# Kernel optimization log

Measured on AMD Instinct MI355X. Metric: run time of the kernel, lower is better.

The kernel has to match this reference:

```python
import jax, jax.numpy as jnp
import numpy as np

B, N, D, H, E = 128, 256, 256, 8, 524288
RATIO = 0.5
HD = D // H
K_SEL = int(N * RATIO)  # nodes kept per graph


def setup_inputs() -> dict:
    key = jax.random.key(0)
    ks = jax.random.split(key, 12)
    embeddings = jax.random.normal(ks[0], (B, N, D), dtype=jnp.float32)
    mask = jnp.ones((B, N), dtype=bool)
    dist = jax.random.uniform(ks[1], (B, N, N), dtype=jnp.float32)
    # within-graph random edges, offset per graph
    epg = E // B
    src = jax.random.randint(ks[2], (B, epg), 0, N)
    dst = jax.random.randint(ks[3], (B, epg), 0, N)
    off = (jnp.arange(B) * N)[:, None]
    edge_index = jnp.stack([(src + off).reshape(-1), (dst + off).reshape(-1)]).astype(jnp.int64)
    batch = jnp.repeat(jnp.arange(B, dtype=jnp.int64), N)
    s = 1.0 / np.sqrt(D)
    Wq = jax.random.normal(ks[4], (D, D), jnp.float32) * s
    Wk = jax.random.normal(ks[5], (D, D), jnp.float32) * s
    Wv = jax.random.normal(ks[6], (D, D), jnp.float32) * s
    Wo = jax.random.normal(ks[7], (D, D), jnp.float32) * s
    bq = jnp.zeros((D,), jnp.float32)
    bk = jnp.zeros((D,), jnp.float32)
    bv = jnp.zeros((D,), jnp.float32)
    bo = jnp.zeros((D,), jnp.float32)
    pool_w = jax.random.normal(ks[8], (D,), jnp.float32) * s
    return dict(embeddings=embeddings, mask=mask, dist=dist, edge_index=edge_index,
                batch=batch, Wq=Wq, bq=bq, Wk=Wk, bk=bk, Wv=Wv, bv=bv, Wo=Wo, bo=bo,
                pool_w=pool_w)


def _mha(x, mask, dist, Wq, bq, Wk, bk, Wv, bv, Wo, bo):
    # x: [B,N,D]; dist used as additive attention bias; mask: [B,N] key mask
    q = (x @ Wq + bq).reshape(B, N, H, HD).transpose(0, 2, 1, 3)  # bhnd
    k = (x @ Wk + bk).reshape(B, N, H, HD).transpose(0, 2, 1, 3)
    v = (x @ Wv + bv).reshape(B, N, H, HD).transpose(0, 2, 1, 3)
    scores = jnp.einsum('bhnd,bhmd->bhnm', q, k) / jnp.sqrt(jnp.float32(HD))
    scores = scores + dist[:, None]  # broadcast bias over heads
    scores = jnp.where(mask[:, None, None, :], scores, jnp.float32(-1e9))
    attn = jax.nn.softmax(scores, axis=-1)
    out = jnp.einsum('bhnm,bhmd->bhnd', attn, v)
    out = out.transpose(0, 2, 1, 3).reshape(B, N, D)
    return out @ Wo + bo


def reference(embeddings, mask, dist, edge_index, batch, Wq, bq, Wk, bk, Wv, bv, Wo, bo, pool_w):
    encoder_result = _mha(embeddings, mask, dist, Wq, bq, Wk, bk, Wv, bv, Wo, bo)
    # encoder_result[mask] -> sparse node features; mask is all-true so shape is [B*N, D]
    x = encoder_result.reshape(B * N, D)

    # ---- TopKPooling (PyG semantics): score = x.w/||w||, keep top ceil(ratio*N)/graph ----
    score = (x @ pool_w) / jnp.linalg.norm(pool_w)          # [B*N]
    vals, idx = jax.lax.top_k(score.reshape(B, N), K_SEL)    # per-graph top-k
    perm = (idx + (jnp.arange(B) * N)[:, None]).reshape(-1)  # [B*K] global node ids
    sub_x = x[perm] * jnp.tanh(vals).reshape(-1, 1)
    sub_batch = batch[perm]

    # relabel nodes: new id = position in perm (PyG ordering); dropped -> sentinel
    n_keep = B * K_SEL
    sentinel = n_keep
    new_id = jnp.full((B * N,), sentinel, dtype=edge_index.dtype).at[perm].set(
        jnp.arange(n_keep, dtype=edge_index.dtype))
    row = new_id[edge_index[0]]
    col = new_id[edge_index[1]]
    valid = (row < sentinel) & (col < sentinel)
    row = jnp.where(valid, row, sentinel)
    col = jnp.where(valid, col, sentinel)
    # sort_edge_index: row-major sort; invalid (sentinel) edges pushed to the end
    order = jnp.argsort(row * (sentinel + 1) + col)
    sub_edge_index = jnp.stack([row, col])[:, order]
    return encoder_result, sub_x, sub_edge_index, sub_batch
```

## Files before the change

### kernel.cpp

```cpp
#include <hip/hip_runtime.h>
#include <math.h>

#define Bg   128
#define Ng   256
#define Dg   256
#define Hg   8
#define HDg  32
#define Eg   524288
#define Kg   128
#define BNg  32768
#define SENT 16384

using bf16x8 = __attribute__((ext_vector_type(8))) short;
using f32x4  = __attribute__((ext_vector_type(4))) float;

__device__ inline void split2(float x, short &h, short &l) {
    unsigned u = __float_as_uint(x);
    h = (short)(u >> 16);
    float hf = __uint_as_float(u & 0xffff0000u);
    float r = x - hf;
    l = (short)(__float_as_uint(r) >> 16);
}
__device__ inline unsigned packsplit(float x) {
    unsigned u = __float_as_uint(x);
    float hf = __uint_as_float(u & 0xffff0000u);
    float r = x - hf;
    unsigned lu = __float_as_uint(r);
    return (u >> 16) | (lu & 0xffff0000u);
}
__device__ inline unsigned pack2(short a, short b) {
    return (unsigned)(unsigned short)a | ((unsigned)(unsigned short)b << 16);
}

__global__ __launch_bounds__(256) void split_x(
    const float* __restrict__ x, short* __restrict__ xh, short* __restrict__ xl)
{
    size_t i = ((size_t)blockIdx.x * 256 + threadIdx.x) * 8;
    float4 a = *(const float4*)(x + i);
    float4 b = *(const float4*)(x + i + 4);
    float v[8] = {a.x,a.y,a.z,a.w,b.x,b.y,b.z,b.w};
    short h[8], l[8];
    #pragma unroll
    for (int j = 0; j < 8; ++j) split2(v[j], h[j], l[j]);
    uint4 uh, ul;
    uh.x = pack2(h[0],h[1]); uh.y = pack2(h[2],h[3]);
    uh.z = pack2(h[4],h[5]); uh.w = pack2(h[6],h[7]);
    ul.x = pack2(l[0],l[1]); ul.y = pack2(l[2],l[3]);
    ul.z = pack2(l[4],l[5]); ul.w = pack2(l[6],l[7]);
    *(uint4*)(xh + i) = uh;
    *(uint4*)(xl + i) = ul;
}

__global__ __launch_bounds__(256) void wprep(
    const float* __restrict__ Wq, const float* __restrict__ Wk,
    const float* __restrict__ Wv, const float* __restrict__ Wo,
    short* __restrict__ WTh, short* __restrict__ WTl)
{
    __shared__ float t[64][65];
    const int bid = blockIdx.x;
    const int mat = bid >> 4;
    const int kt = (bid >> 2) & 3, nt = bid & 3;
    const float* W = (mat==0) ? Wq : (mat==1) ? Wk : (mat==2) ? Wv : Wo;
    const int tid = threadIdx.x;
    const int r = tid >> 2, c4 = tid & 3;
    #pragma unroll
    for (int i = 0; i < 4; ++i) {
        float4 v = *(const float4*)(W + (size_t)(kt*64 + r)*256 + nt*64 + c4*16 + i*4);
        t[r][c4*16 + i*4 + 0] = v.x; t[r][c4*16 + i*4 + 1] = v.y;
        t[r][c4*16 + i*4 + 2] = v.z; t[r][c4*16 + i*4 + 3] = v.w;
    }
    __syncthreads();
    const int n = r, k0 = c4 * 16;
    short hb[16], lb[16];
    #pragma unroll
    for (int i = 0; i < 16; ++i) split2(t[k0 + i][n], hb[i], lb[i]);
    size_t base = (size_t)mat*65536 + (size_t)(nt*64 + n)*256 + kt*64 + k0;
    uint4 uh0, uh1, ul0, ul1;
    uh0.x=pack2(hb[0],hb[1]);  uh0.y=pack2(hb[2],hb[3]);  uh0.z=pack2(hb[4],hb[5]);  uh0.w=pack2(hb[6],hb[7]);
    uh1.x=pack2(hb[8],hb[9]);  uh1.y=pack2(hb[10],hb[11]);uh1.z=pack2(hb[12],hb[13]);uh1.w=pack2(hb[14],hb[15]);
    ul0.x=pack2(lb[0],lb[1]);  ul0.y=pack2(lb[2],lb[3]);  ul0.z=pack2(lb[4],lb[5]);  ul0.w=pack2(lb[6],lb[7]);
    ul1.x=pack2(lb[8],lb[9]);  ul1.y=pack2(lb[10],lb[11]);ul1.z=pack2(lb[12],lb[13]);ul1.w=pack2(lb[14],lb[15]);
    *(uint4*)&WTh[base]     = uh0; *(uint4*)&WTh[base + 8] = uh1;
    *(uint4*)&WTl[base]     = ul0; *(uint4*)&WTl[base + 8] = ul1;
}

__global__ __launch_bounds__(256) void qkv_mm(
    const short* __restrict__ xh, const short* __restrict__ xl,
    const short* __restrict__ WTh, const short* __restrict__ WTl,
    const float* __restrict__ bq, const float* __restrict__ bk, const float* __restrict__ bv,
    float* __restrict__ Qo, float* __restrict__ Ko, float* __restrict__ Vo)
{
    const int z = blockIdx.z;
    const float* bias = (z==0) ? bq : (z==1) ? bk : bv;
    float* out        = (z==0) ? Qo : (z==1) ? Ko : Vo;
    const short* bth = WTh + (size_t)z * 65536;
    const short* btl = WTl + (size_t)z * 65536;
    __shared__ __align__(16) short lds[16384];
    const int tid = threadIdx.x;
    const int lane = tid & 63, w = tid >> 6;
    const int g = lane >> 4, li = lane & 15;
    const int wr = w >> 1, wc = w & 1;
    const int m0 = blockIdx.x * 128, n0 = blockIdx.y * 128;
    f32x4 acc[4][4];
    #pragma unroll
    for (int i = 0; i < 4; ++i)
        #pragma unroll
        for (int j = 0; j < 4; ++j) acc[i][j] = (f32x4){0.f,0.f,0.f,0.f};

    for (int k0 = 0; k0 < 256; k0 += 32) {
        #pragma unroll
        for (int it = 0; it < 2; ++it) {
            int chunk = it*256 + tid;
            int r = chunk >> 2, c = chunk & 3;
            size_t ga = (size_t)(m0 + r)*256 + k0 + c*8;
            size_t gb = (size_t)(n0 + r)*256 + k0 + c*8;
            uint4 vh = *(const uint4*)(xh + ga);
            uint4 vl = *(const uint4*)(xl + ga);
            uint4 wh = *(const uint4*)(bth + gb);
            uint4 wl = *(const uint4*)(btl + gb);
            *(uint4*)&lds[        chunk*8] = vh;
            *(uint4*)&lds[ 4096 + chunk*8] = vl;
            *(uint4*)&lds[ 8192 + chunk*8] = wh;
            *(uint4*)&lds[12288 + chunk*8] = wl;
        }
        __syncthreads();
        bf16x8 ah[4], al[4], bh[4], bl[4];
        #pragma unroll
        for (int i = 0; i < 4; ++i) {
            int row = wr*64 + i*16 + li;
            ah[i] = *(const bf16x8*)&lds[       row*32 + g*8];
            al[i] = *(const bf16x8*)&lds[4096 + row*32 + g*8];
        }
        #pragma unroll
        for (int j = 0; j < 4; ++j) {
            int row = wc*64 + j*16 + li;
            bh[j] = *(const bf16x8*)&lds[ 8192 + row*32 + g*8];
            bl[j] = *(const bf16x8*)&lds[12288 + row*32 + g*8];
        }
        #pragma unroll
        for (int i = 0; i < 4; ++i)
            #pragma unroll
            for (int j = 0; j < 4; ++j) {
                acc[i][j] = __builtin_amdgcn_mfma_f32_16x16x32_bf16(ah[i], bh[j], acc[i][j], 0,0,0);
                acc[i][j] = __builtin_amdgcn_mfma_f32_16x16x32_bf16(ah[i], bl[j], acc[i][j], 0,0,0);
                acc[i][j] = __builtin_amdgcn_mfma_f32_16x16x32_bf16(al[i], bh[j], acc[i][j], 0,0,0);
                acc[i][j] = __builtin_amdgcn_mfma_f32_16x16x32_bf16(al[i], bl[j], acc[i][j], 0,0,0);
            }
        __syncthreads();
    }
    #pragma unroll
    for (int i = 0; i < 4; ++i)
        #pragma unroll
        for (int j = 0; j < 4; ++j)
            #pragma unroll
            for (int r = 0; r < 4; ++r) {
                int m = m0 + wr*64 + i*16 + g*4 + r;
                int c = n0 + wc*64 + j*16 + li;
                int b = m >> 8, nn = m & 255;
                int h = c >> 5, hd = c & 31;
                out[((size_t)(b*Hg + h)*Ng + nn)*HDg + hd] = acc[i][j][r] + bias[c];
            }
}

__global__ __launch_bounds__(256) void attn_mfma(
    const float* Qf, const float* __restrict__ Kx,
    const float* __restrict__ Vx, const float* __restrict__ dist,
    short* __restrict__ AOh, short* __restrict__ AOl)
{
    __shared__ short    Khi[2][32][40];
    __shared__ short    Klo[2][32][40];
    __shared__ unsigned Vt [2][32][36];
    __shared__ unsigned P32[4][64][36];

    const int bh = blockIdx.x;
    const int b  = bh >> 3;
    const int h  = bh & 7;
    const int tid = threadIdx.x;
    const int w = tid >> 6;
    const int lane = tid & 63;
    const int g = lane >> 4;
    const int li = lane & 15;
    const int q0 = w * 64;

    bf16x8 qh[4], ql[4];
    #pragma unroll
    for (int tq = 0; tq < 4; ++tq) {
        const float* qp = Qf + ((size_t)bh * Ng + q0 + tq*16 + li) * HDg + g*8;
        float4 qa = *(const float4*)qp;
        float4 qb = *(const float4*)(qp + 4);
        float v[8] = {qa.x,qa.y,qa.z,qa.w,qb.x,qb.y,qb.z,qb.w};
        #pragma unroll
        for (int j = 0; j < 8; ++j) {
            short hh,ll; split2(v[j] * 0.17677669529663687f, hh, ll);
            qh[tq][j] = hh; ql[tq][j] = ll;
        }
    }

    {
        int key = tid >> 3, e0 = (tid & 7) * 4;
        float4 kv = *(const float4*)(Kx + ((size_t)bh*Ng + key) * HDg + e0);
        float4 vv = *(const float4*)(Vx + ((size_t)bh*Ng + key) * HDg + e0);
        float ka[4] = {kv.x,kv.y,kv.z,kv.w}, va[4] = {vv.x,vv.y,vv.z,vv.w};
        #pragma unroll
        for (int i = 0; i < 4; ++i) {
            short hh,ll; split2(ka[i], hh, ll);
            Khi[0][key][e0+i] = hh; Klo[0][key][e0+i] = ll;
            Vt[0][e0+i][key] = packsplit(va[i]);
        }
    }
    __syncthreads();

    f32x4 O[4][2];
    #pragma unroll
    for (int tq=0;tq<4;++tq)
        #pragma unroll
        for (int td=0;td<2;++td) O[tq][td] = (f32x4){0.f,0.f,0.f,0.f};
    float lpart[4][4] = {};

    for (int ch = 0; ch < 8; ++ch) {
        const int cur = ch & 1;
        if (ch < 7) {
            int key = tid >> 3, e0 = (tid & 7) * 4;
            float4 kv = *(const float4*)(Kx + ((size_t)bh*Ng + (ch+1)*32 + key) * HDg + e0);
            float4 vv = *(const float4*)(Vx + ((size_t)bh*Ng + (ch+1)*32 + key) * HDg + e0);
            float ka[4]={kv.x,kv.y,kv.z,kv.w}, va[4]={vv.x,vv.y,vv.z,vv.w};
            int nb = cur ^ 1;
            #pragma unroll
            for (int i = 0; i < 4; ++i) {
                short hh,ll; split2(ka[i], hh, ll);
                Khi[nb][key][e0+i] = hh; Klo[nb][key][e0+i] = ll;
                Vt[nb][e0+i][key] = packsplit(va[i]);
            }
        }
        f32x4 sacc[4][2];
        const float* dbase = dist + (size_t)b*Ng*Ng + ch*32;
        #pragma unroll
        for (int tq = 0; tq < 4; ++tq)
            #pragma unroll
            for (int tc = 0; tc < 2; ++tc) {
                const float* dp = dbase + (size_t)(q0 + tq*16 + g*4)*Ng + tc*16 + li;
                f32x4 s;
                s[0]=dp[0]; s[1]=dp[Ng]; s[2]=dp[2*Ng]; s[3]=dp[3*Ng];
                sacc[tq][tc] = s;
            }
        bf16x8 kbh[2], kbl[2];
        #pragma unroll
        for (int tc = 0; tc < 2; ++tc) {
            kbh[tc] = *(const bf16x8*)&Khi[cur][tc*16+li][g*8];
            kbl[tc] = *(const bf16x8*)&Klo[cur][tc*16+li][g*8];
        }
        #pragma unroll
        for (int tq = 0; tq < 4; ++tq)
            #pragma unroll
            for (int tc = 0; tc < 2; ++tc) {
                sacc[tq][tc] = __builtin_amdgcn_mfma_f32_16x16x32_bf16(qh[tq], kbh[tc], sacc[tq][tc], 0,0,0);
                sacc[tq][tc] = __builtin_amdgcn_mfma_f32_16x16x32_bf16(qh[tq], kbl[tc], sacc[tq][tc], 0,0,0);
                sacc[tq][tc] = __builtin_amdgcn_mfma_f32_16x16x32_bf16(ql[tq], kbh[tc], sacc[tq][tc], 0,0,0);
                sacc[tq][tc] = __builtin_amdgcn_mfma_f32_16x16x32_bf16(ql[tq], kbl[tc], sacc[tq][tc], 0,0,0);
            }
        #pragma unroll
        for (int tq = 0; tq < 4; ++tq)
            #pragma unroll
            for (int tc = 0; tc < 2; ++tc)
                #pragma unroll
                for (int r = 0; r < 4; ++r) {
                    float p = __expf(sacc[tq][tc][r] - 16.f);
                    lpart[tq][r] += p;
                    P32[w][tq*16 + g*4 + r][tc*16 + li] = packsplit(p);
                }
        __syncthreads();
        bf16x8 vbh[2], vbl[2];
        #pragma unroll
        for (int td = 0; td < 2; ++td) {
            unsigned tmp[8];
            *(uint4*)&tmp[0] = *(const uint4*)&Vt[cur][td*16+li][g*8];
            *(uint4*)&tmp[4] = *(const uint4*)&Vt[cur][td*16+li][g*8+4];
            #pragma unroll
            for (int j=0;j<8;++j){ vbh[td][j]=(short)(tmp[j]&0xffff); vbl[td][j]=(short)(tmp[j]>>16); }
        }
        #pragma unroll
        for (int tq = 0; tq < 4; ++tq) {
            unsigned tmp[8];
            *(uint4*)&tmp[0] = *(const uint4*)&P32[w][tq*16+li][g*8];
            *(uint4*)&tmp[4] = *(const uint4*)&P32[w][tq*16+li][g*8+4];
            bf16x8 ph, pl;
            #pragma unroll
            for (int j=0;j<8;++j){ ph[j]=(short)(tmp[j]&0xffff); pl[j]=(short)(tmp[j]>>16); }
            #pragma unroll
            for (int td = 0; td < 2; ++td) {
                O[tq][td] = __builtin_amdgcn_mfma_f32_16x16x32_bf16(ph, vbh[td], O[tq][td], 0,0,0);
                O[tq][td] = __builtin_amdgcn_mfma_f32_16x16x32_bf16(ph, vbl[td], O[tq][td], 0,0,0);
                O[tq][td] = __builtin_amdgcn_mfma_f32_16x16x32_bf16(pl, vbh[td], O[tq][td], 0,0,0);
                O[tq][td] = __builtin_amdgcn_mfma_f32_16x16x32_bf16(pl, vbl[td], O[tq][td], 0,0,0);
            }
        }
        __syncthreads();
    }
    #pragma unroll
    for (int tq = 0; tq < 4; ++tq)
        #pragma unroll
        for (int r = 0; r < 4; ++r) {
            float s = lpart[tq][r];
            s += __shfl_xor(s, 1); s += __shfl_xor(s, 2);
            s += __shfl_xor(s, 4); s += __shfl_xor(s, 8);
            lpart[tq][r] = 1.f / s;
        }
    #pragma unroll
    for (int tq = 0; tq < 4; ++tq)
        #pragma unroll
        for (int td = 0; td < 2; ++td)
            #pragma unroll
            for (int r = 0; r < 4; ++r) {
                int q = q0 + tq*16 + g*4 + r;
                float val = O[tq][td][r] * lpart[tq][r];
                short hh, ll; split2(val, hh, ll);
                size_t idx = ((size_t)b*Ng + q)*Dg + h*HDg + td*16 + li;
                AOh[idx] = hh; AOl[idx] = ll;
            }
}

__global__ __launch_bounds__(256) void out_mm(
    const short* __restrict__ ah_g, const short* __restrict__ al_g,
    const short* __restrict__ bth, const short* __restrict__ btl,
    const float* __restrict__ bo, float* __restrict__ enc)
{
    __shared__ __align__(16) short lds[16384];
    const int tid = threadIdx.x;
    const int lane = tid & 63, w = tid >> 6;
    const int g = lane >> 4, li = lane & 15;
    const int wr = w >> 1, wc = w & 1;
    const int m0 = blockIdx.x * 128, n0 = blockIdx.y * 128;
    f32x4 acc[4][4];
    #pragma unroll
    for (int i = 0; i < 4; ++i)
        #pragma unroll
        for (int j = 0; j < 4; ++j) acc[i][j] = (f32x4){0.f,0.f,0.f,0.f};

    for (int k0 = 0; k0 < 256; k0 += 32) {
        #pragma unroll
        for (int it = 0; it < 2; ++it) {
            int chunk = it*256 + tid;
            int r = chunk >> 2, c = chunk & 3;
            size_t ga = (size_t)(m0 + r)*256 + k0 + c*8;
            size_t gb = (size_t)(n0 + r)*256 + k0 + c*8;
            uint4 vh = *(const uint4*)(ah_g + ga);
            uint4 vl = *(const uint4*)(al_g + ga);
            uint4 wh = *(const uint4*)(bth + gb);
            uint4 wl = *(const uint4*)(btl + gb);
            *(uint4*)&lds[        chunk*8] = vh;
            *(uint4*)&lds[ 4096 + chunk*8] = vl;
            *(uint4*)&lds[ 8192 + chunk*8] = wh;
            *(uint4*)&lds[12288 + chunk*8] = wl;
        }
        __syncthreads();
        bf16x8 ah[4], al[4], bh[4], bl[4];
        #pragma unroll
        for (int i = 0; i < 4; ++i) {
            int row = wr*64 + i*16 + li;
            ah[i] = *(const bf16x8*)&lds[       row*32 + g*8];
            al[i] = *(const bf16x8*)&lds[4096 + row*32 + g*8];
        }
        #pragma unroll
        for (int j = 0; j < 4; ++j) {
            int row = wc*64 + j*16 + li;
            bh[j] = *(const bf16x8*)&lds[ 8192 + row*32 + g*8];
            bl[j] = *(const bf16x8*)&lds[12288 + row*32 + g*8];
        }
        #pragma unroll
        for (int i = 0; i < 4; ++i)
            #pragma unroll
            for (int j = 0; j < 4; ++j) {
                acc[i][j] = __builtin_amdgcn_mfma_f32_16x16x32_bf16(ah[i], bh[j], acc[i][j], 0,0,0);
                acc[i][j] = __builtin_amdgcn_mfma_f32_16x16x32_bf16(ah[i], bl[j], acc[i][j], 0,0,0);
                acc[i][j] = __builtin_amdgcn_mfma_f32_16x16x32_bf16(al[i], bh[j], acc[i][j], 0,0,0);
                acc[i][j] = __builtin_amdgcn_mfma_f32_16x16x32_bf16(al[i], bl[j], acc[i][j], 0,0,0);
            }
        __syncthreads();
    }
    #pragma unroll
    for (int i = 0; i < 4; ++i)
        #pragma unroll
        for (int j = 0; j < 4; ++j)
            #pragma unroll
            for (int r = 0; r < 4; ++r) {
                int m = m0 + wr*64 + i*16 + g*4 + r;
                int c = n0 + wc*64 + j*16 + li;
                enc[(size_t)m*Dg + c] = acc[i][j][r] + bo[c];
            }
}

__global__ __launch_bounds__(256) void score_kernel(
    const float* __restrict__ enc, const float* __restrict__ pw, float* __restrict__ score)
{
    int row  = blockIdx.x * 8 + (threadIdx.x >> 5);
    int lane = threadIdx.x & 31;
    const float* r = enc + (size_t)row * Dg;
    float s = 0.f;
    for (int d = lane; d < Dg; d += 32) s = fmaf(r[d], pw[d], s);
    #pragma unroll
    for (int off = 16; off > 0; off >>= 1) s += __shfl_xor(s, off);
    if (lane == 0) score[row] = s;
}

__global__ void norm_kernel(const float* __restrict__ pw, float* __restrict__ inv_norm)
{
    int t = threadIdx.x;
    float s = 0.f;
    for (int d = t; d < Dg; d += 64) s = fmaf(pw[d], pw[d], s);
    #pragma unroll
    for (int off = 32; off > 0; off >>= 1) s += __shfl_xor(s, off);
    if (t == 0) *inv_norm = 1.0f / sqrtf(s);
}

__global__ __launch_bounds__(256) void topk_kernel(
    const float* __restrict__ score, float* __restrict__ vals, int* __restrict__ idxs,
    int* __restrict__ new_id, float* __restrict__ out_batch)
{
    __shared__ float sh[Ng];
    int bgr = blockIdx.x, t = threadIdx.x;
    float mine = score[(size_t)bgr * Ng + t];
    sh[t] = mine;
    __syncthreads();
    int cnt = 0;
    for (int j = 0; j < Ng; ++j) {
        float v = sh[j];
        cnt += (v > mine || (v == mine && j < t)) ? 1 : 0;
    }
    if (cnt < Kg) {
        int pos = bgr * Kg + cnt;
        vals[pos] = mine;
        idxs[pos] = t;
        new_id[bgr * Ng + t] = pos;
        out_batch[pos] = (float)bgr;
    } else {
        new_id[bgr * Ng + t] = SENT;
    }
}

__global__ __launch_bounds__(256) void subx_kernel(
    const float* __restrict__ enc, const float* __restrict__ vals,
    const int* __restrict__ idxs, const float* __restrict__ inv_norm,
    float* __restrict__ out_subx)
{
    int j    = blockIdx.x * 4 + (threadIdx.x >> 6);
    int lane = threadIdx.x & 63;
    int bgr  = j >> 7;
    int src  = bgr * Ng + idxs[j];
    float scale = tanhf(vals[j] * (*inv_norm));
    float4 v = reinterpret_cast<const float4*>(enc + (size_t)src * Dg)[lane];
    v.x *= scale; v.y *= scale; v.z *= scale; v.w *= scale;
    reinterpret_cast<float4*>(out_subx + (size_t)j * Dg)[lane] = v;
}

__global__ __launch_bounds__(256) void edge_hist(
    const int* __restrict__ ei, const int* __restrict__ new_id, int* __restrict__ counts)
{
    int e = blockIdx.x * 256 + threadIdx.x;
    int r = new_id[ei[e]];
    int c = new_id[ei[Eg + e]];
    if (r != SENT && c != SENT) atomicAdd(&counts[r], 1);
}

__global__ __launch_bounds__(256) void scan_kernel(
    const int* __restrict__ counts, int* __restrict__ offsets)
{
    __shared__ int sums[256];
    int t = threadIdx.x;
    int base = t * 64;
    int s = 0;
    for (int i = 0; i < 64; ++i) s += counts[base + i];
    sums[t] = s;
    __syncthreads();
    for (int off = 1; off < 256; off <<= 1) {
        int add = (t >= off) ? sums[t - off] : 0;
        __syncthreads();
        sums[t] += add;
        __syncthreads();
    }
    int run = sums[t] - s;
    for (int i = 0; i < 64; ++i) { offsets[base + i] = run; run += counts[base + i]; }
    if (t == 255) offsets[SENT] = run;
}

__global__ __launch_bounds__(256) void edge_scatter(
    const int* __restrict__ ei, const int* __restrict__ new_id,
    const int* __restrict__ offsets, int* __restrict__ cursor, int* __restrict__ bucket)
{
    int e = blockIdx.x * 256 + threadIdx.x;
    int r = new_id[ei[e]];
    int c = new_id[ei[Eg + e]];
    if (r != SENT && c != SENT) {
        int pos = offsets[r] + atomicAdd(&cursor[r], 1);
        bucket[pos] = c;
    }
}

__global__ __launch_bounds__(256) void edge_sort_emit(
    const int* __restrict__ offsets, int* bucket, float* __restrict__ out_edges)
{
    int r = blockIdx.x * 256 + threadIdx.x;
    int s = offsets[r], e = offsets[r + 1];
    for (int i = s + 1; i < e; ++i) {
        int key = bucket[i];
        int j = i - 1;
        while (j >= s && bucket[j] > key) { bucket[j+1] = bucket[j]; --j; }
        bucket[j+1] = key;
    }
    float rf = (float)r;
    for (int i = s; i < e; ++i) {
        out_edges[i]      = rf;
        out_edges[Eg + i] = (float)bucket[i];
    }
}

__global__ __launch_bounds__(256) void edge_fill(
    const int* __restrict__ offsets, float* __restrict__ out_edges)
{
    int p = blockIdx.x * 256 + threadIdx.x;
    if (p >= offsets[SENT]) {
        out_edges[p]      = (float)SENT;
        out_edges[Eg + p] = (float)SENT;
    }
}

extern "C" void kernel_launch(void* const* d_in, const int* in_sizes, int n_in,
                              void* d_out, int out_size, void* d_ws, size_t ws_size,
                              hipStream_t stream)
{
    const float* x    = (const float*)d_in[0];
    const float* dist = (const float*)d_in[2];
    const int*   ei   = (const int*)d_in[3];
    const float* Wq = (const float*)d_in[5];
    const float* bq = (const float*)d_in[6];
    const float* Wk = (const float*)d_in[7];
    const float* bk = (const float*)d_in[8];
    const float* Wv = (const float*)d_in[9];
    const float* bv = (const float*)d_in[10];
    const float* Wo = (const float*)d_in[11];
    const float* bo = (const float*)d_in[12];
    const float* pw = (const float*)d_in[13];

    float* out       = (float*)d_out;
    float* enc_out   = out;
    float* subx_out  = out + 8388608;
    float* edge_out  = out + 12582912;
    float* batch_out = out + 13631488;

    float* ws     = (float*)d_ws;
    float* Q      = ws;
    float* Kx     = ws + 8388608;
    float* Vx     = ws + 16777216;
    short* xh     = (short*)(ws + 25165824);
    short* xl     = (short*)(ws + 29360128);
    short* AOh    = xh;
    short* AOl    = xl;
    short* WTh    = (short*)(ws + 33554432);
    short* WTl    = (short*)(ws + 33685504);
    float* score  = ws + 33816576;
    float* vals   = ws + 33849344;
    int*   idxs   = (int*)(ws + 33865728);
    int*   new_id = (int*)(ws + 33882112);
    int*   counts = (int*)(ws + 33914880);
    int*   offsets= (int*)(ws + 33931264);
    int*   cursor = (int*)(ws + 33947680);
    float* inv_nm = ws + 33964064;
    int*   bucket = (int*)(ws + 33964096);

    hipMemsetAsync(counts, 0, SENT * sizeof(int), stream);
    hipMemsetAsync(cursor, 0, SENT * sizeof(int), stream);

    split_x       <<<dim3(4096),               256, 0, stream>>>(x, xh, xl);
    wprep         <<<dim3(64),                 256, 0, stream>>>(Wq, Wk, Wv, Wo, WTh, WTl);
    norm_kernel   <<<dim3(1),                   64, 0, stream>>>(pw, inv_nm);
    qkv_mm        <<<dim3(BNg/128, Dg/128, 3), 256, 0, stream>>>(xh, xl, WTh, WTl, bq, bk, bv, Q, Kx, Vx);
    attn_mfma     <<<dim3(Bg*Hg),              256, 0, stream>>>(Q, Kx, Vx, dist, AOh, AOl);
    out_mm        <<<dim3(BNg/128, Dg/128),    256, 0, stream>>>(AOh, AOl, WTh + 3*65536, WTl + 3*65536, bo, enc_out);
    score_kernel  <<<dim3(BNg/8),              256, 0, stream>>>(enc_out, pw, score);
    topk_kernel   <<<dim3(Bg),                 256, 0, stream>>>(score, vals, idxs, new_id, batch_out);
    subx_kernel   <<<dim3((Bg*Kg)/4),          256, 0, stream>>>(enc_out, vals, idxs, inv_nm, subx_out);
    edge_hist     <<<dim3(Eg/256),             256, 0, stream>>>(ei, new_id, counts);
    scan_kernel   <<<dim3(1),                  256, 0, stream>>>(counts, offsets);
    edge_scatter  <<<dim3(Eg/256),             256, 0, stream>>>(ei, new_id, offsets, cursor, bucket);
    edge_sort_emit<<<dim3(SENT/256),           256, 0, stream>>>(offsets, bucket, edge_out);
    edge_fill     <<<dim3(Eg/256),             256, 0, stream>>>(offsets, edge_out);
    (void)in_sizes; (void)n_in; (void)out_size; (void)ws_size;
}
```

Before: 242.5 us.

## Emit pre-split bf16 hi/lo Q/K/V from GEMM and shrink attention P staging

The QKV GEMM now folds the query scale into its epilogue and writes each value as a packed bf16 hi/lo pair. The attention kernel therefore loads these packed words directly instead of re-splitting fp32 values per block. The attention output is also written as packed pairs that out_mm unpacks on load. The per-warp P staging buffer shrinks to one 16-row tile reused per query tile, which removes a block-wide barrier per chunk, lowers LDS use, and adds a launch bound that asks for 4 blocks per SM. The cost is unpacking work inside out_mm and possible extra register pressure from the occupancy bound.

```diff
diff --git a/kernel.cpp b/kernel.cpp
--- a/kernel.cpp
+++ b/kernel.cpp
@@ -88,11 +88,12 @@
     const short* __restrict__ xh, const short* __restrict__ xl,
     const short* __restrict__ WTh, const short* __restrict__ WTl,
     const float* __restrict__ bq, const float* __restrict__ bk, const float* __restrict__ bv,
-    float* __restrict__ Qo, float* __restrict__ Ko, float* __restrict__ Vo)
+    unsigned* __restrict__ Qp, unsigned* __restrict__ Kp, unsigned* __restrict__ Vp)
 {
     const int z = blockIdx.z;
     const float* bias = (z==0) ? bq : (z==1) ? bk : bv;
-    float* out        = (z==0) ? Qo : (z==1) ? Ko : Vo;
+    unsigned* out     = (z==0) ? Qp : (z==1) ? Kp : Vp;
+    const float scale = (z==0) ? 0.17677669529663687f : 1.0f;
     const short* bth = WTh + (size_t)z * 65536;
     const short* btl = WTl + (size_t)z * 65536;
     __shared__ __align__(16) short lds[16384];
@@ -158,19 +159,20 @@
                 int c = n0 + wc*64 + j*16 + li;
                 int b = m >> 8, nn = m & 255;
                 int h = c >> 5, hd = c & 31;
-                out[((size_t)(b*Hg + h)*Ng + nn)*HDg + hd] = acc[i][j][r] + bias[c];
-            }
-}
-
-__global__ __launch_bounds__(256) void attn_mfma(
-    const float* Qf, const float* __restrict__ Kx,
-    const float* __restrict__ Vx, const float* __restrict__ dist,
-    short* __restrict__ AOh, short* __restrict__ AOl)
+                float val = (acc[i][j][r] + bias[c]) * scale;
+                out[((size_t)(b*Hg + h)*Ng + nn)*HDg + hd] = packsplit(val);
+            }
+}
+
+__global__ __launch_bounds__(256, 4) void attn_mfma(
+    const unsigned* __restrict__ Qp, const unsigned* __restrict__ Kp,
+    const unsigned* __restrict__ Vp, const float* __restrict__ dist,
+    unsigned* __restrict__ AOp)
 {
     __shared__ short    Khi[2][32][40];
     __shared__ short    Klo[2][32][40];
     __shared__ unsigned Vt [2][32][36];
-    __shared__ unsigned P32[4][64][36];
+    __shared__ unsigned Pw [4][16][36];
 
     const int bh = blockIdx.x;
     const int b  = bh >> 3;
@@ -185,27 +187,28 @@
     bf16x8 qh[4], ql[4];
     #pragma unroll
     for (int tq = 0; tq < 4; ++tq) {
-        const float* qp = Qf + ((size_t)bh * Ng + q0 + tq*16 + li) * HDg + g*8;
-        float4 qa = *(const float4*)qp;
-        float4 qb = *(const float4*)(qp + 4);
-        float v[8] = {qa.x,qa.y,qa.z,qa.w,qb.x,qb.y,qb.z,qb.w};
+        const unsigned* qp = Qp + ((size_t)bh * Ng + q0 + tq*16 + li) * HDg + g*8;
+        uint4 u0 = *(const uint4*)qp;
+        uint4 u1 = *(const uint4*)(qp + 4);
+        unsigned uu[8] = {u0.x,u0.y,u0.z,u0.w,u1.x,u1.y,u1.z,u1.w};
         #pragma unroll
         for (int j = 0; j < 8; ++j) {
-            short hh,ll; split2(v[j] * 0.17677669529663687f, hh, ll);
-            qh[tq][j] = hh; ql[tq][j] = ll;
+            qh[tq][j] = (short)(uu[j] & 0xffff);
+            ql[tq][j] = (short)(uu[j] >> 16);
         }
     }
 
     {
         int key = tid >> 3, e0 = (tid & 7) * 4;
-        float4 kv = *(const float4*)(Kx + ((size_t)bh*Ng + key) * HDg + e0);
-        float4 vv = *(const float4*)(Vx + ((size_t)bh*Ng + key) * HDg + e0);
-        float ka[4] = {kv.x,kv.y,kv.z,kv.w}, va[4] = {vv.x,vv.y,vv.z,vv.w};
+        uint4 kv = *(const uint4*)(Kp + ((size_t)bh*Ng + key) * HDg + e0);
+        uint4 vv = *(const uint4*)(Vp + ((size_t)bh*Ng + key) * HDg + e0);
+        unsigned ka[4] = {kv.x,kv.y,kv.z,kv.w};
+        unsigned va[4] = {vv.x,vv.y,vv.z,vv.w};
         #pragma unroll
         for (int i = 0; i < 4; ++i) {
-            short hh,ll; split2(ka[i], hh, ll);
-            Khi[0][key][e0+i] = hh; Klo[0][key][e0+i] = ll;
-            Vt[0][e0+i][key] = packsplit(va[i]);
+            Khi[0][key][e0+i] = (short)(ka[i] & 0xffff);
+            Klo[0][key][e0+i] = (short)(ka[i] >> 16);
+            Vt [0][e0+i][key] = va[i];
         }
     }
     __syncthreads();
@@ -221,15 +224,16 @@
         const int cur = ch & 1;
         if (ch < 7) {
             int key = tid >> 3, e0 = (tid & 7) * 4;
-            float4 kv = *(const float4*)(Kx + ((size_t)bh*Ng + (ch+1)*32 + key) * HDg + e0);
-            float4 vv = *(const float4*)(Vx + ((size_t)bh*Ng + (ch+1)*32 + key) * HDg + e0);
-            float ka[4]={kv.x,kv.y,kv.z,kv.w}, va[4]={vv.x,vv.y,vv.z,vv.w};
+            uint4 kv = *(const uint4*)(Kp + ((size_t)bh*Ng + (ch+1)*32 + key) * HDg + e0);
+            uint4 vv = *(const uint4*)(Vp + ((size_t)bh*Ng + (ch+1)*32 + key) * HDg + e0);
+            unsigned ka[4] = {kv.x,kv.y,kv.z,kv.w};
+            unsigned va[4] = {vv.x,vv.y,vv.z,vv.w};
             int nb = cur ^ 1;
             #pragma unroll
             for (int i = 0; i < 4; ++i) {
-                short hh,ll; split2(ka[i], hh, ll);
-                Khi[nb][key][e0+i] = hh; Klo[nb][key][e0+i] = ll;
-                Vt[nb][e0+i][key] = packsplit(va[i]);
+                Khi[nb][key][e0+i] = (short)(ka[i] & 0xffff);
+                Klo[nb][key][e0+i] = (short)(ka[i] >> 16);
+                Vt [nb][e0+i][key] = va[i];
             }
         }
         f32x4 sacc[4][2];
@@ -258,31 +262,28 @@
                 sacc[tq][tc] = __builtin_amdgcn_mfma_f32_16x16x32_bf16(ql[tq], kbh[tc], sacc[tq][tc], 0,0,0);
                 sacc[tq][tc] = __builtin_amdgcn_mfma_f32_16x16x32_bf16(ql[tq], kbl[tc], sacc[tq][tc], 0,0,0);
             }
-        #pragma unroll
-        for (int tq = 0; tq < 4; ++tq)
+        bf16x8 vbh[2], vbl[2];
+        #pragma unroll
+        for (int td = 0; td < 2; ++td) {
+            unsigned tmp[8];
+            *(uint4*)&tmp[0] = *(const uint4*)&Vt[cur][td*16+li][g*8];
+            *(uint4*)&tmp[4] = *(const uint4*)&Vt[cur][td*16+li][g*8+4];
+            #pragma unroll
+            for (int j=0;j<8;++j){ vbh[td][j]=(short)(tmp[j]&0xffff); vbl[td][j]=(short)(tmp[j]>>16); }
+        }
+        #pragma unroll
+        for (int tq = 0; tq < 4; ++tq) {
             #pragma unroll
             for (int tc = 0; tc < 2; ++tc)
                 #pragma unroll
                 for (int r = 0; r < 4; ++r) {
                     float p = __expf(sacc[tq][tc][r] - 16.f);
                     lpart[tq][r] += p;
-                    P32[w][tq*16 + g*4 + r][tc*16 + li] = packsplit(p);
+                    Pw[w][g*4 + r][tc*16 + li] = packsplit(p);
                 }
-        __syncthreads();
-        bf16x8 vbh[2], vbl[2];
-        #pragma unroll
-        for (int td = 0; td < 2; ++td) {
             unsigned tmp[8];
-            *(uint4*)&tmp[0] = *(const uint4*)&Vt[cur][td*16+li][g*8];
-            *(uint4*)&tmp[4] = *(const uint4*)&Vt[cur][td*16+li][g*8+4];
-            #pragma unroll
-            for (int j=0;j<8;++j){ vbh[td][j]=(short)(tmp[j]&0xffff); vbl[td][j]=(short)(tmp[j]>>16); }
-        }
-        #pragma unroll
-        for (int tq = 0; tq < 4; ++tq) {
-            unsigned tmp[8];
-            *(uint4*)&tmp[0] = *(const uint4*)&P32[w][tq*16+li][g*8];
-            *(uint4*)&tmp[4] = *(const uint4*)&P32[w][tq*16+li][g*8+4];
+            *(uint4*)&tmp[0] = *(const uint4*)&Pw[w][li][g*8];
+            *(uint4*)&tmp[4] = *(const uint4*)&Pw[w][li][g*8+4];
             bf16x8 ph, pl;
             #pragma unroll
             for (int j=0;j<8;++j){ ph[j]=(short)(tmp[j]&0xffff); pl[j]=(short)(tmp[j]>>16); }
@@ -313,14 +314,12 @@
             for (int r = 0; r < 4; ++r) {
                 int q = q0 + tq*16 + g*4 + r;
                 float val = O[tq][td][r] * lpart[tq][r];
-                short hh, ll; split2(val, hh, ll);
-                size_t idx = ((size_t)b*Ng + q)*Dg + h*HDg + td*16 + li;
-                AOh[idx] = hh; AOl[idx] = ll;
+                AOp[((size_t)b*Ng + q)*Dg + h*HDg + td*16 + li] = packsplit(val);
             }
 }
 
 __global__ __launch_bounds__(256) void out_mm(
-    const short* __restrict__ ah_g, const short* __restrict__ al_g,
+    const unsigned* __restrict__ aop,
     const short* __restrict__ bth, const short* __restrict__ btl,
     const float* __restrict__ bo, float* __restrict__ enc)
 {
@@ -343,12 +342,18 @@
             int r = chunk >> 2, c = chunk & 3;
             size_t ga = (size_t)(m0 + r)*256 + k0 + c*8;
             size_t gb = (size_t)(n0 + r)*256 + k0 + c*8;
-            uint4 vh = *(const uint4*)(ah_g + ga);
-            uint4 vl = *(const uint4*)(al_g + ga);
+            uint4 p0 = *(const uint4*)(aop + ga);
+            uint4 p1 = *(const uint4*)(aop + ga + 4);
+            unsigned a[8] = {p0.x,p0.y,p0.z,p0.w,p1.x,p1.y,p1.z,p1.w};
+            uint4 hw, lw;
+            hw.x = (a[0]&0xffffu)|(a[1]<<16); lw.x = (a[0]>>16)|(a[1]&0xffff0000u);
+            hw.y = (a[2]&0xffffu)|(a[3]<<16); lw.y = (a[2]>>16)|(a[3]&0xffff0000u);
+            hw.z = (a[4]&0xffffu)|(a[5]<<16); lw.z = (a[4]>>16)|(a[5]&0xffff0000u);
+            hw.w = (a[6]&0xffffu)|(a[7]<<16); lw.w = (a[6]>>16)|(a[7]&0xffff0000u);
             uint4 wh = *(const uint4*)(bth + gb);
             uint4 wl = *(const uint4*)(btl + gb);
-            *(uint4*)&lds[        chunk*8] = vh;
-            *(uint4*)&lds[ 4096 + chunk*8] = vl;
+            *(uint4*)&lds[        chunk*8] = hw;
+            *(uint4*)&lds[ 4096 + chunk*8] = lw;
             *(uint4*)&lds[ 8192 + chunk*8] = wh;
             *(uint4*)&lds[12288 + chunk*8] = wl;
         }
@@ -546,25 +551,24 @@
     float* edge_out  = out + 12582912;
     float* batch_out = out + 13631488;
 
-    float* ws     = (float*)d_ws;
-    float* Q      = ws;
-    float* Kx     = ws + 8388608;
-    float* Vx     = ws + 16777216;
-    short* xh     = (short*)(ws + 25165824);
-    short* xl     = (short*)(ws + 29360128);
-    short* AOh    = xh;
-    short* AOl    = xl;
-    short* WTh    = (short*)(ws + 33554432);
-    short* WTl    = (short*)(ws + 33685504);
-    float* score  = ws + 33816576;
-    float* vals   = ws + 33849344;
-    int*   idxs   = (int*)(ws + 33865728);
-    int*   new_id = (int*)(ws + 33882112);
-    int*   counts = (int*)(ws + 33914880);
-    int*   offsets= (int*)(ws + 33931264);
-    int*   cursor = (int*)(ws + 33947680);
-    float* inv_nm = ws + 33964064;
-    int*   bucket = (int*)(ws + 33964096);
+    float* ws      = (float*)d_ws;
+    unsigned* Qp   = (unsigned*)ws;
+    unsigned* Kp   = (unsigned*)(ws + 8388608);
+    unsigned* Vp   = (unsigned*)(ws + 16777216);
+    short* xh      = (short*)(ws + 25165824);
+    short* xl      = (short*)(ws + 29360128);
+    unsigned* AOp  = (unsigned*)xh;
+    short* WTh     = (short*)(ws + 33554432);
+    short* WTl     = (short*)(ws + 33685504);
+    float* score   = ws + 33816576;
+    float* vals    = ws + 33849344;
+    int*   idxs    = (int*)(ws + 33865728);
+    int*   new_id  = (int*)(ws + 33882112);
+    int*   counts  = (int*)(ws + 33914880);
+    int*   offsets = (int*)(ws + 33931264);
+    int*   cursor  = (int*)(ws + 33947680);
+    float* inv_nm  = ws + 33964064;
+    int*   bucket  = (int*)(ws + 33964096);
 
     hipMemsetAsync(counts, 0, SENT * sizeof(int), stream);
     hipMemsetAsync(cursor, 0, SENT * sizeof(int), stream);
@@ -572,9 +576,9 @@
     split_x       <<<dim3(4096),               256, 0, stream>>>(x, xh, xl);
     wprep         <<<dim3(64),                 256, 0, stream>>>(Wq, Wk, Wv, Wo, WTh, WTl);
     norm_kernel   <<<dim3(1),                   64, 0, stream>>>(pw, inv_nm);
-    qkv_mm        <<<dim3(BNg/128, Dg/128, 3), 256, 0, stream>>>(xh, xl, WTh, WTl, bq, bk, bv, Q, Kx, Vx);
-    attn_mfma     <<<dim3(Bg*Hg),              256, 0, stream>>>(Q, Kx, Vx, dist, AOh, AOl);
-    out_mm        <<<dim3(BNg/128, Dg/128),    256, 0, stream>>>(AOh, AOl, WTh + 3*65536, WTl + 3*65536, bo, enc_out);
+    qkv_mm        <<<dim3(BNg/128, Dg/128, 3), 256, 0, stream>>>(xh, xl, WTh, WTl, bq, bk, bv, Qp, Kp, Vp);
+    attn_mfma     <<<dim3(Bg*Hg),              256, 0, stream>>>(Qp, Kp, Vp, dist, AOp);
+    out_mm        <<<dim3(BNg/128, Dg/128),    256, 0, stream>>>(AOp, WTh + 3*65536, WTl + 3*65536, bo, enc_out);
     score_kernel  <<<dim3(BNg/8),              256, 0, stream>>>(enc_out, pw, score);
     topk_kernel   <<<dim3(Bg),                 256, 0, stream>>>(score, vals, idxs, new_id, batch_out);
     subx_kernel   <<<dim3((Bg*Kg)/4),          256, 0, stream>>>(enc_out, vals, idxs, inv_nm, subx_out);
```

Measured after the change: 277.6 us. +14.4%, slower.
